# Kernel optimization log

Hardware: AMD Instinct MI355X
Metric: run time of the kernel (lower is better)

Reference implementation:

```python
import jax, jax.numpy as jnp
import numpy as np

DIM = 384
NUM_HEADS = 6
HEAD_SIZE = DIM // NUM_HEADS


def setup_inputs() -> dict:
    key = jax.random.key(0)
    k1, k2, k3, k4, k5 = jax.random.split(key, 5)
    x = jax.random.normal(k1, (2, 4096, DIM), dtype=jnp.float32)
    # qkv Linear(dim, 3*dim): weight [3*dim, dim], bias [3*dim] (torch layout)
    w_qkv = jax.random.normal(k2, (3 * DIM, DIM), dtype=jnp.float32) * (1.0 / np.sqrt(DIM))
    b_qkv = jax.random.normal(k3, (3 * DIM,), dtype=jnp.float32) * 1e-6
    w_proj = jax.random.normal(k4, (DIM, DIM), dtype=jnp.float32) * (1.0 / np.sqrt(DIM))
    b_proj = jax.random.normal(k5, (DIM,), dtype=jnp.float32) * 0.01
    return {"x": x, "w_qkv": w_qkv, "b_qkv": b_qkv, "w_proj": w_proj, "b_proj": b_proj}


def reference(x, w_qkv, b_qkv, w_proj, b_proj):
    B, N, C = x.shape
    H, D = NUM_HEADS, HEAD_SIZE
    # qkv projection: [B, N, 3C]
    qkv = jnp.einsum("bnc,fc->bnf", x, w_qkv) + b_qkv
    # view(B, N, 3, H, D) -> permute to (3, B, H, N, D)
    qkv = qkv.reshape(B, N, 3, H, D).transpose(2, 0, 3, 1, 4)
    q, k, v = qkv[0], qkv[1], qkv[2]
    # full attention matrix [B, H, N, N] (matches the naive module)
    att = jnp.einsum("bhnd,bhmd->bhnm", q, k) / jnp.sqrt(jnp.float32(D)).astype(x.dtype)
    att = jax.nn.softmax(att, axis=-1)  # attn_drop p=0 -> identity
    out = jnp.einsum("bhnm,bhmd->bhnd", att, v)  # [B, H, N, D]
    out = out.transpose(0, 2, 1, 3).reshape(B, N, C)
    out = jnp.einsum("bnc,fc->bnf", out, w_proj) + b_proj  # proj_drop p=0 -> identity
    return out
```

## Files before the change

kernel.cpp:

```cpp
#include <hip/hip_runtime.h>
#include <stdint.h>

#define DIM   384
#define NH    6
#define SEQ   4096
#define MTOT  (2*SEQ)

typedef __bf16 bf16x8 __attribute__((ext_vector_type(8)));
typedef float  f32x4  __attribute__((ext_vector_type(4)));
typedef unsigned short u16;
typedef u16 u16x4 __attribute__((ext_vector_type(4)));
typedef u16 u16x8 __attribute__((ext_vector_type(8)));
typedef uint32_t u32x4 __attribute__((ext_vector_type(4)));

extern "C" __device__ float __ocml_native_exp2_f32(float);

__device__ __forceinline__ u16 f2b(float f) {
  uint32_t u = __builtin_bit_cast(uint32_t, f);
  u += 0x7fffu + ((u >> 16) & 1u);
  return (u16)(u >> 16);
}

#define GLDS16(gp, lp) \
  __builtin_amdgcn_global_load_lds((const __attribute__((address_space(1))) void*)(gp), \
                                   (__attribute__((address_space(3))) void*)(lp), 16, 0, 0)

__global__ void conv_bf16_all(const float* __restrict__ x, const float* __restrict__ wq,
                              const float* __restrict__ wp, u16* __restrict__ xb,
                              u16* __restrict__ wqb, u16* __restrict__ wpb) {
  int i = blockIdx.x * 256 + threadIdx.x;
  const float* src; u16* dst; int off;
  if (i < 393216)      { src = x;  dst = xb;  off = i; }
  else if (i < 448512) { src = wq; dst = wqb; off = i - 393216; }
  else                 { src = wp; dst = wpb; off = i - 448512; }
  float4 a = ((const float4*)src)[2*off];
  float4 b = ((const float4*)src)[2*off+1];
  u16x8 r;
  r[0]=f2b(a.x); r[1]=f2b(a.y); r[2]=f2b(a.z); r[3]=f2b(a.w);
  r[4]=f2b(b.x); r[5]=f2b(b.y); r[6]=f2b(b.z); r[7]=f2b(b.w);
  ((u16x8*)dst)[off] = r;
}

template<int EPI>
__global__ __launch_bounds__(256) void gemm_bt_kernel(
    const u16* __restrict__ A,
    const u16* __restrict__ Bw,
    const float* __restrict__ bias,
    u16* __restrict__ Qb, u16* __restrict__ Kb, u16* __restrict__ Vt,
    float* __restrict__ Out)
{
  __shared__ u16 As[2][64*64];
  __shared__ u16 Bs[2][96*64];
  const int tid = threadIdx.x;
  const int wid = tid >> 6, lane = tid & 63;
  const int lr = lane & 15, lg = lane >> 4;
  const int m0 = blockIdx.x * 64;
  const int f0 = blockIdx.y * 96;
  const int wm = (wid >> 1) * 32, wn = (wid & 1) * 48;
  const f32x4 z4 = {0.f, 0.f, 0.f, 0.f};
  f32x4 acc[2][3];
  #pragma unroll
  for (int i = 0; i < 2; ++i)
    #pragma unroll
    for (int j = 0; j < 3; ++j) acc[i][j] = z4;

  auto stage = [&](int k, int buf) {
    const int k0 = k * 64;
    #pragma unroll
    for (int i = 0; i < 2; ++i) {
      const int wb  = i*4096 + wid*1024;
      const int ob  = wb + lane*16;
      const int row = ob >> 7;
      const int lch = ((ob >> 4) & 7) ^ (row & 7);
      GLDS16(A + (size_t)(m0+row)*384 + k0 + lch*8, &As[buf][0] + wb/2);
    }
    #pragma unroll
    for (int i = 0; i < 3; ++i) {
      const int wb  = i*4096 + wid*1024;
      const int ob  = wb + lane*16;
      const int row = ob >> 7;
      const int lch = ((ob >> 4) & 7) ^ (row & 7);
      GLDS16(Bw + (size_t)(f0+row)*384 + k0 + lch*8, &Bs[buf][0] + wb/2);
    }
  };

  stage(0, 0);
  #pragma unroll
  for (int k = 0; k < 6; ++k) {
    const int cur = k & 1;
    if (k < 5) {
      stage(k+1, cur ^ 1);
      asm volatile("s_waitcnt vmcnt(5)" ::: "memory");
    } else {
      asm volatile("s_waitcnt vmcnt(0)" ::: "memory");
    }
    __builtin_amdgcn_s_barrier();
    asm volatile("" ::: "memory");
    #pragma unroll
    for (int ks = 0; ks < 2; ++ks) {
      bf16x8 af[2], bfr[3];
      #pragma unroll
      for (int mi = 0; mi < 2; ++mi) {
        int r = wm + mi*16 + lr;
        af[mi] = *(const bf16x8*)(&As[cur][0] + (r*128 + ((ks*64 + lg*16) ^ ((r&7)<<4)))/2);
      }
      #pragma unroll
      for (int ni = 0; ni < 3; ++ni) {
        int r = wn + ni*16 + lr;
        bfr[ni] = *(const bf16x8*)(&Bs[cur][0] + (r*128 + ((ks*64 + lg*16) ^ ((r&7)<<4)))/2);
      }
      #pragma unroll
      for (int mi = 0; mi < 2; ++mi)
        #pragma unroll
        for (int ni = 0; ni < 3; ++ni)
          acc[mi][ni] = __builtin_amdgcn_mfma_f32_16x16x32_bf16(af[mi], bfr[ni], acc[mi][ni], 0, 0, 0);
    }
    __builtin_amdgcn_s_barrier();
    asm volatile("" ::: "memory");
  }

  if (EPI == 0) {
    const int which = f0 / 384;
    #pragma unroll
    for (int ni = 0; ni < 3; ++ni) {
      const int f   = f0 + wn + ni*16 + lr;
      const float bv = bias[f];
      const int rem = f - which*384;
      const int h = rem >> 6, d = rem & 63;
      #pragma unroll
      for (int mi = 0; mi < 2; ++mi) {
        const int m = m0 + wm + mi*16 + lg*4;
        const int b = m >> 12, n = m & 4095;
        const size_t bh = (size_t)(b*NH + h);
        if (which == 0) {
          #pragma unroll
          for (int j = 0; j < 4; ++j)
            Qb[(bh*SEQ + n + j)*64 + d] = f2b((acc[mi][ni][j] + bv) * 0.1803368801111244f);
        } else if (which == 1) {
          #pragma unroll
          for (int j = 0; j < 4; ++j)
            Kb[(bh*SEQ + n + j)*64 + d] = f2b(acc[mi][ni][j] + bv);
        } else {
          u16x4 pk;
          #pragma unroll
          for (int j = 0; j < 4; ++j) pk[j] = f2b(acc[mi][ni][j] + bv);
          *(u16x4*)(Vt + (bh*64 + d)*SEQ + n) = pk;
        }
      }
    }
  } else {
    #pragma unroll
    for (int ni = 0; ni < 3; ++ni) {
      const int f = f0 + wn + ni*16 + lr;
      const float bv = bias[f];
      #pragma unroll
      for (int mi = 0; mi < 2; ++mi) {
        const int m = m0 + wm + mi*16 + lg*4;
        #pragma unroll
        for (int j = 0; j < 4; ++j)
          Out[(size_t)(m+j)*DIM + f] = acc[mi][ni][j] + bv;
      }
    }
  }
}

__global__ __launch_bounds__(256, 3) void attn_kernel(
    const u16* __restrict__ Qb, const u16* __restrict__ Kb, const u16* __restrict__ Vt,
    u16* __restrict__ AO)
{
  __shared__ uint32_t smem[8192];
  char* sb = (char*)smem;
  const int tid = threadIdx.x;
  const int wid = tid >> 6, lane = tid & 63;
  const int lr = lane & 15, lg = lane >> 4;
  const int id = blockIdx.y * 64 + blockIdx.x;
  const int w  = (id & 7) * 96 + (id >> 3);
  const int bh = w >> 6;
  const int q0 = (w & 63) * 64;
  const u16* Qp = Qb + (size_t)bh*SEQ*64;
  const u16* Kp = Kb + (size_t)bh*SEQ*64;
  const u16* Vp = Vt + (size_t)bh*64*SEQ;

  bf16x8 qf[2];
  #pragma unroll
  for (int ks = 0; ks < 2; ++ks)
    qf[ks] = *(const bf16x8*)(Qp + (size_t)(q0 + wid*16 + lr)*64 + ks*32 + lg*8);

  bf16x8 onesf;
  {
    u32x4 ow = {0x3F803F80u, 0x3F803F80u, 0x3F803F80u, 0x3F803F80u};
    onesf = __builtin_bit_cast(bf16x8, ow);
  }

  const int la0 = lr*128 + ((lg*16) ^ ((lr&7)<<4));
  const int la1 = la0 ^ 64;

  const int r0  = tid >> 3;
  const int lch = (tid & 7) ^ (r0 & 7);
  const u16* kS  = Kp + r0*64 + lch*8;
  const u16* vS  = Vp + (size_t)r0*SEQ + lch*8;
  const u16* vS2 = Vp + (size_t)(r0+32)*SEQ + lch*8;
  char* kD = sb + tid*16;
  char* vD = sb + 16384 + tid*16;

  const f32x4 z4 = {0.f,0.f,0.f,0.f};
  f32x4 o[4] = {z4, z4, z4, z4};
  f32x4 ol = z4;
  f32x4 sA[4], sB[4];

  auto QK = [&](f32x4 (&s)[4], int KR) {
    __builtin_amdgcn_s_setprio(1);
    #pragma unroll
    for (int ni = 0; ni < 4; ++ni) {
      bf16x8 k0 = *(const bf16x8*)(sb + KR + ni*2048 + la0);
      bf16x8 k1 = *(const bf16x8*)(sb + KR + ni*2048 + la1);
      s[ni] = __builtin_amdgcn_mfma_f32_16x16x32_bf16(k0, qf[0], z4, 0, 0, 0);
      s[ni] = __builtin_amdgcn_mfma_f32_16x16x32_bf16(k1, qf[1], s[ni], 0, 0, 0);
    }
    __builtin_amdgcn_s_setprio(0);
  };

  auto SM_PV = [&](f32x4 (&s)[4], int VR) {
    #pragma unroll
    for (int ni = 0; ni < 4; ++ni)
      #pragma unroll
      for (int j = 0; j < 4; ++j)
        s[ni][j] = __ocml_native_exp2_f32(s[ni][j]);
    bf16x8 pf[2];
    #pragma unroll
    for (int ks = 0; ks < 2; ++ks) {
      uint32_t A, B, C, D;
      asm("v_cvt_pk_bf16_f32 %0, %1, %2" : "=v"(A) : "v"(s[2*ks][0]),   "v"(s[2*ks][1]));
      asm("v_cvt_pk_bf16_f32 %0, %1, %2" : "=v"(B) : "v"(s[2*ks][2]),   "v"(s[2*ks][3]));
      asm("v_cvt_pk_bf16_f32 %0, %1, %2" : "=v"(C) : "v"(s[2*ks+1][0]), "v"(s[2*ks+1][1]));
      asm("v_cvt_pk_bf16_f32 %0, %1, %2" : "=v"(D) : "v"(s[2*ks+1][2]), "v"(s[2*ks+1][3]));
      asm("v_permlane32_swap_b32 %0, %1" : "+v"(A), "+v"(C));
      asm("v_permlane16_swap_b32 %0, %1" : "+v"(A), "+v"(C));
      asm("v_permlane32_swap_b32 %0, %1" : "+v"(B), "+v"(D));
      asm("v_permlane16_swap_b32 %0, %1" : "+v"(B), "+v"(D));
      u32x4 wv = {A, B, C, D};
      pf[ks] = __builtin_bit_cast(bf16x8, wv);
    }
    __builtin_amdgcn_s_setprio(1);
    #pragma unroll
    for (int df = 0; df < 4; ++df) {
      bf16x8 v0 = *(const bf16x8*)(sb + 16384 + VR + df*2048 + la0);
      bf16x8 v1 = *(const bf16x8*)(sb + 16384 + VR + df*2048 + la1);
      o[df] = __builtin_amdgcn_mfma_f32_16x16x32_bf16(pf[0], v0, o[df], 0, 0, 0);
      o[df] = __builtin_amdgcn_mfma_f32_16x16x32_bf16(pf[1], v1, o[df], 0, 0, 0);
    }
    ol = __builtin_amdgcn_mfma_f32_16x16x32_bf16(pf[0], onesf, ol, 0, 0, 0);
    ol = __builtin_amdgcn_mfma_f32_16x16x32_bf16(pf[1], onesf, ol, 0, 0, 0);
    __builtin_amdgcn_s_setprio(0);
  };

  GLDS16(kS, kD);                 GLDS16(kS + 2048, kD + 4096);
  GLDS16(kS + 4096, kD + 8192);   GLDS16(kS + 4096 + 2048, kD + 8192 + 4096);
  GLDS16(vS, vD);                 GLDS16(vS2, vD + 4096);
  asm volatile("s_waitcnt vmcnt(0)" ::: "memory");
  __builtin_amdgcn_s_barrier();
  asm volatile("" ::: "memory");
  QK(sA, 0);
  __builtin_amdgcn_s_barrier();
  asm volatile("" ::: "memory");

  for (int t = 0; t < 62; t += 2) {
    GLDS16(kS + (t+2)*4096, kD);             GLDS16(kS + (t+2)*4096 + 2048, kD + 4096);
    GLDS16(vS + (t+1)*64, vD + 8192);        GLDS16(vS2 + (t+1)*64, vD + 8192 + 4096);
    QK(sB, 8192);
    SM_PV(sA, 0);
    asm volatile("s_waitcnt vmcnt(0)" ::: "memory");
    __builtin_amdgcn_s_barrier();
    asm volatile("" ::: "memory");
    GLDS16(kS + (t+3)*4096, kD + 8192);      GLDS16(kS + (t+3)*4096 + 2048, kD + 8192 + 4096);
    GLDS16(vS + (t+2)*64, vD);               GLDS16(vS2 + (t+2)*64, vD + 4096);
    QK(sA, 0);
    SM_PV(sB, 8192);
    asm volatile("s_waitcnt vmcnt(0)" ::: "memory");
    __builtin_amdgcn_s_barrier();
    asm volatile("" ::: "memory");
  }
  GLDS16(vS + 63*64, vD + 8192);             GLDS16(vS2 + 63*64, vD + 8192 + 4096);
  QK(sB, 8192);
  SM_PV(sA, 0);
  asm volatile("s_waitcnt vmcnt(0)" ::: "memory");
  __builtin_amdgcn_s_barrier();
  asm volatile("" ::: "memory");
  SM_PV(sB, 8192);

  const int b = bh / NH, h = bh - b*NH;
  float linv[4];
  #pragma unroll
  for (int j = 0; j < 4; ++j) linv[j] = 1.f / ol[j];
  #pragma unroll
  for (int df = 0; df < 4; ++df)
    #pragma unroll
    for (int j = 0; j < 4; ++j) {
      const int n = q0 + wid*16 + lg*4 + j;
      AO[((size_t)(b*SEQ + n))*DIM + h*64 + df*16 + lr] = f2b(o[df][j] * linv[j]);
    }
}

extern "C" void kernel_launch(void* const* d_in, const int* in_sizes, int n_in,
                              void* d_out, int out_size, void* d_ws, size_t ws_size,
                              hipStream_t stream) {
  const float* x      = (const float*)d_in[0];
  const float* w_qkv  = (const float*)d_in[1];
  const float* b_qkv  = (const float*)d_in[2];
  const float* w_proj = (const float*)d_in[3];
  const float* b_proj = (const float*)d_in[4];
  float* out = (float*)d_out;
  char* ws = (char*)d_ws;

  u16* xb  = (u16*)(ws);
  u16* wqb = (u16*)(ws + 6291456);
  u16* wpb = (u16*)(ws + 7176192);
  u16* Qb  = (u16*)(ws + 7471104);
  u16* Kb  = (u16*)(ws + 13762560);
  u16* Vt  = (u16*)(ws + 20054016);
  u16* AO  = (u16*)(ws + 26345472);

  conv_bf16_all<<<dim3(1824), dim3(256), 0, stream>>>(x, w_qkv, w_proj, xb, wqb, wpb);
  gemm_bt_kernel<0><<<dim3(MTOT/64, (3*DIM)/96), dim3(256), 0, stream>>>(
      xb, wqb, b_qkv, Qb, Kb, Vt, nullptr);
  attn_kernel<<<dim3(SEQ/64, 2*NH), dim3(256), 0, stream>>>(Qb, Kb, Vt, AO);
  gemm_bt_kernel<1><<<dim3(MTOT/64, DIM/96), dim3(256), 0, stream>>>(
      AO, wpb, b_proj, nullptr, nullptr, nullptr, out);
}
```

Baseline: 97.60 us.

## Fuse fp32-to-bf16 conversion of x into QKV GEMM loading A directly to registers

Removes the separate conversion pass over the activations: the QKV GEMM now reads fp32 x straight from global memory into registers, packs it to bf16 with v_cvt_pk_bf16_f32, and feeds MFMA without staging A in LDS. The conversion kernel now handles only the weights. This saves a full write and reread of a bf16 copy of x. In exchange, each block rereads fp32 rows of x across the output-column blocks, doubling the bytes per A load, and relies on hand-tuned vmcnt waits. The projection GEMM is split out as its own non-templated kernel.

```diff
diff --git a/kernel.cpp b/kernel.cpp
--- a/kernel.cpp
+++ b/kernel.cpp
@@ -25,14 +25,12 @@
   __builtin_amdgcn_global_load_lds((const __attribute__((address_space(1))) void*)(gp), \
                                    (__attribute__((address_space(3))) void*)(lp), 16, 0, 0)
 
-__global__ void conv_bf16_all(const float* __restrict__ x, const float* __restrict__ wq,
-                              const float* __restrict__ wp, u16* __restrict__ xb,
-                              u16* __restrict__ wqb, u16* __restrict__ wpb) {
+__global__ void conv_bf16_w(const float* __restrict__ wq, const float* __restrict__ wp,
+                            u16* __restrict__ wqb, u16* __restrict__ wpb) {
   int i = blockIdx.x * 256 + threadIdx.x;
   const float* src; u16* dst; int off;
-  if (i < 393216)      { src = x;  dst = xb;  off = i; }
-  else if (i < 448512) { src = wq; dst = wqb; off = i - 393216; }
-  else                 { src = wp; dst = wpb; off = i - 448512; }
+  if (i < 55296) { src = wq; dst = wqb; off = i; }
+  else           { src = wp; dst = wpb; off = i - 55296; }
   float4 a = ((const float4*)src)[2*off];
   float4 b = ((const float4*)src)[2*off+1];
   u16x8 r;
@@ -41,12 +39,129 @@
   ((u16x8*)dst)[off] = r;
 }
 
-template<int EPI>
-__global__ __launch_bounds__(256) void gemm_bt_kernel(
+__device__ __forceinline__ uint32_t cvtpk(float lo, float hi) {
+  uint32_t r;
+  asm("v_cvt_pk_bf16_f32 %0, %1, %2" : "=v"(r) : "v"(lo), "v"(hi));
+  return r;
+}
+
+__global__ __launch_bounds__(256, 6) void gemm_qkv_kernel(
+    const float* __restrict__ X,
+    const u16* __restrict__ Bw,
+    const float* __restrict__ bias,
+    u16* __restrict__ Qb, u16* __restrict__ Kb, u16* __restrict__ Vt)
+{
+  __shared__ u16 Bs[2][96*64];
+  const int tid = threadIdx.x;
+  const int wid = tid >> 6, lane = tid & 63;
+  const int lr = lane & 15, lg = lane >> 4;
+  const int m0 = blockIdx.x * 64;
+  const int f0 = blockIdx.y * 96;
+  const int wm = (wid >> 1) * 32, wn = (wid & 1) * 48;
+  const f32x4 z4 = {0.f, 0.f, 0.f, 0.f};
+  f32x4 acc[2][3];
+  #pragma unroll
+  for (int i = 0; i < 2; ++i)
+    #pragma unroll
+    for (int j = 0; j < 3; ++j) acc[i][j] = z4;
+
+  const char* xr0 = (const char*)(X + (size_t)(m0 + wm + lr)*384 + lg*8);
+  const char* xr1 = (const char*)(X + (size_t)(m0 + wm + 16 + lr)*384 + lg*8);
+
+  auto stageB = [&](int k, int buf) {
+    const int k0 = k * 64;
+    #pragma unroll
+    for (int i = 0; i < 3; ++i) {
+      const int wb  = i*4096 + wid*1024;
+      const int ob  = wb + lane*16;
+      const int row = ob >> 7;
+      const int lch = ((ob >> 4) & 7) ^ (row & 7);
+      GLDS16(Bw + (size_t)(f0+row)*384 + k0 + lch*8, &Bs[buf][0] + wb/2);
+    }
+  };
+
+  stageB(0, 0);
+  #pragma unroll
+  for (int k = 0; k < 6; ++k) {
+    const int cur = k & 1;
+    float4 a00 = *(const float4*)(xr0 + k*256);
+    float4 a01 = *(const float4*)(xr0 + k*256 + 16);
+    float4 a10 = *(const float4*)(xr1 + k*256);
+    float4 a11 = *(const float4*)(xr1 + k*256 + 16);
+    asm volatile("s_waitcnt vmcnt(4)" ::: "memory");
+    __builtin_amdgcn_s_barrier();
+    asm volatile("" ::: "memory");
+    if (k < 5) stageB(k+1, cur ^ 1);
+    float4 b00 = *(const float4*)(xr0 + k*256 + 128);
+    float4 b01 = *(const float4*)(xr0 + k*256 + 144);
+    float4 b10 = *(const float4*)(xr1 + k*256 + 128);
+    float4 b11 = *(const float4*)(xr1 + k*256 + 144);
+    if (k < 5) { asm volatile("s_waitcnt vmcnt(7)" ::: "memory"); }
+    else       { asm volatile("s_waitcnt vmcnt(4)" ::: "memory"); }
+    {
+      u32x4 w0 = {cvtpk(a00.x,a00.y), cvtpk(a00.z,a00.w), cvtpk(a01.x,a01.y), cvtpk(a01.z,a01.w)};
+      u32x4 w1 = {cvtpk(a10.x,a10.y), cvtpk(a10.z,a10.w), cvtpk(a11.x,a11.y), cvtpk(a11.z,a11.w)};
+      bf16x8 af0 = __builtin_bit_cast(bf16x8, w0);
+      bf16x8 af1 = __builtin_bit_cast(bf16x8, w1);
+      #pragma unroll
+      for (int ni = 0; ni < 3; ++ni) {
+        int r = wn + ni*16 + lr;
+        bf16x8 bfr = *(const bf16x8*)(&Bs[cur][0] + (r*128 + ((lg*16) ^ ((r&7)<<4)))/2);
+        acc[0][ni] = __builtin_amdgcn_mfma_f32_16x16x32_bf16(af0, bfr, acc[0][ni], 0, 0, 0);
+        acc[1][ni] = __builtin_amdgcn_mfma_f32_16x16x32_bf16(af1, bfr, acc[1][ni], 0, 0, 0);
+      }
+    }
+    if (k < 5) { asm volatile("s_waitcnt vmcnt(3)" ::: "memory"); }
+    else       { asm volatile("s_waitcnt vmcnt(0)" ::: "memory"); }
+    {
+      u32x4 w0 = {cvtpk(b00.x,b00.y), cvtpk(b00.z,b00.w), cvtpk(b01.x,b01.y), cvtpk(b01.z,b01.w)};
+      u32x4 w1 = {cvtpk(b10.x,b10.y), cvtpk(b10.z,b10.w), cvtpk(b11.x,b11.y), cvtpk(b11.z,b11.w)};
+      bf16x8 af0 = __builtin_bit_cast(bf16x8, w0);
+      bf16x8 af1 = __builtin_bit_cast(bf16x8, w1);
+      #pragma unroll
+      for (int ni = 0; ni < 3; ++ni) {
+        int r = wn + ni*16 + lr;
+        bf16x8 bfr = *(const bf16x8*)(&Bs[cur][0] + (r*128 + ((64 + lg*16) ^ ((r&7)<<4)))/2);
+        acc[0][ni] = __builtin_amdgcn_mfma_f32_16x16x32_bf16(af0, bfr, acc[0][ni], 0, 0, 0);
+        acc[1][ni] = __builtin_amdgcn_mfma_f32_16x16x32_bf16(af1, bfr, acc[1][ni], 0, 0, 0);
+      }
+    }
+  }
+
+  const int which = f0 / 384;
+  #pragma unroll
+  for (int ni = 0; ni < 3; ++ni) {
+    const int f   = f0 + wn + ni*16 + lr;
+    const float bv = bias[f];
+    const int rem = f - which*384;
+    const int h = rem >> 6, d = rem & 63;
+    #pragma unroll
+    for (int mi = 0; mi < 2; ++mi) {
+      const int m = m0 + wm + mi*16 + lg*4;
+      const int b = m >> 12, n = m & 4095;
+      const size_t bh = (size_t)(b*NH + h);
+      if (which == 0) {
+        #pragma unroll
+        for (int j = 0; j < 4; ++j)
+          Qb[(bh*SEQ + n + j)*64 + d] = f2b((acc[mi][ni][j] + bv) * 0.1803368801111244f);
+      } else if (which == 1) {
+        #pragma unroll
+        for (int j = 0; j < 4; ++j)
+          Kb[(bh*SEQ + n + j)*64 + d] = f2b(acc[mi][ni][j] + bv);
+      } else {
+        u16x4 pk;
+        #pragma unroll
+        for (int j = 0; j < 4; ++j) pk[j] = f2b(acc[mi][ni][j] + bv);
+        *(u16x4*)(Vt + (bh*64 + d)*SEQ + n) = pk;
+      }
+    }
+  }
+}
+
+__global__ __launch_bounds__(256) void gemm_proj_kernel(
     const u16* __restrict__ A,
     const u16* __restrict__ Bw,
     const float* __restrict__ bias,
-    u16* __restrict__ Qb, u16* __restrict__ Kb, u16* __restrict__ Vt,
     float* __restrict__ Out)
 {
   __shared__ u16 As[2][64*64];
@@ -119,47 +234,16 @@
     asm volatile("" ::: "memory");
   }
 
-  if (EPI == 0) {
-    const int which = f0 / 384;
-    #pragma unroll
-    for (int ni = 0; ni < 3; ++ni) {
-      const int f   = f0 + wn + ni*16 + lr;
-      const float bv = bias[f];
-      const int rem = f - which*384;
-      const int h = rem >> 6, d = rem & 63;
-      #pragma unroll
-      for (int mi = 0; mi < 2; ++mi) {
-        const int m = m0 + wm + mi*16 + lg*4;
-        const int b = m >> 12, n = m & 4095;
-        const size_t bh = (size_t)(b*NH + h);
-        if (which == 0) {
-          #pragma unroll
-          for (int j = 0; j < 4; ++j)
-            Qb[(bh*SEQ + n + j)*64 + d] = f2b((acc[mi][ni][j] + bv) * 0.1803368801111244f);
-        } else if (which == 1) {
-          #pragma unroll
-          for (int j = 0; j < 4; ++j)
-            Kb[(bh*SEQ + n + j)*64 + d] = f2b(acc[mi][ni][j] + bv);
-        } else {
-          u16x4 pk;
-          #pragma unroll
-          for (int j = 0; j < 4; ++j) pk[j] = f2b(acc[mi][ni][j] + bv);
-          *(u16x4*)(Vt + (bh*64 + d)*SEQ + n) = pk;
-        }
-      }
-    }
-  } else {
-    #pragma unroll
-    for (int ni = 0; ni < 3; ++ni) {
-      const int f = f0 + wn + ni*16 + lr;
-      const float bv = bias[f];
-      #pragma unroll
-      for (int mi = 0; mi < 2; ++mi) {
-        const int m = m0 + wm + mi*16 + lg*4;
-        #pragma unroll
-        for (int j = 0; j < 4; ++j)
-          Out[(size_t)(m+j)*DIM + f] = acc[mi][ni][j] + bv;
-      }
+  #pragma unroll
+  for (int ni = 0; ni < 3; ++ni) {
+    const int f = f0 + wn + ni*16 + lr;
+    const float bv = bias[f];
+    #pragma unroll
+    for (int mi = 0; mi < 2; ++mi) {
+      const int m = m0 + wm + mi*16 + lg*4;
+      #pragma unroll
+      for (int j = 0; j < 4; ++j)
+        Out[(size_t)(m+j)*DIM + f] = acc[mi][ni][j] + bv;
     }
   }
 }
@@ -312,7 +396,6 @@
   float* out = (float*)d_out;
   char* ws = (char*)d_ws;
 
-  u16* xb  = (u16*)(ws);
   u16* wqb = (u16*)(ws + 6291456);
   u16* wpb = (u16*)(ws + 7176192);
   u16* Qb  = (u16*)(ws + 7471104);
@@ -320,10 +403,10 @@
   u16* Vt  = (u16*)(ws + 20054016);
   u16* AO  = (u16*)(ws + 26345472);
 
-  conv_bf16_all<<<dim3(1824), dim3(256), 0, stream>>>(x, w_qkv, w_proj, xb, wqb, wpb);
-  gemm_bt_kernel<0><<<dim3(MTOT/64, (3*DIM)/96), dim3(256), 0, stream>>>(
-      xb, wqb, b_qkv, Qb, Kb, Vt, nullptr);
+  conv_bf16_w<<<dim3(288), dim3(256), 0, stream>>>(w_qkv, w_proj, wqb, wpb);
+  gemm_qkv_kernel<<<dim3(MTOT/64, (3*DIM)/96), dim3(256), 0, stream>>>(
+      x, wqb, b_qkv, Qb, Kb, Vt);
   attn_kernel<<<dim3(SEQ/64, 2*NH), dim3(256), 0, stream>>>(Qb, Kb, Vt, AO);
-  gemm_bt_kernel<1><<<dim3(MTOT/64, DIM/96), dim3(256), 0, stream>>>(
-      AO, wpb, b_proj, nullptr, nullptr, nullptr, out);
-}
+  gemm_proj_kernel<<<dim3(MTOT/64, DIM/96), dim3(256), 0, stream>>>(
+      AO, wpb, b_proj, out);
+}
```

After: 120.9 us. 1.24x slower.
